# Performance work log

Hardware: AMD Instinct MI355X
Metric: run time of the kernel (lower is better)

The kernel has to match this reference:

```python
import jax, jax.numpy as jnp
import numpy as np

N = 13627
E = 504378
D = 500


def _seg_softmax(e, seg, n):
    m = jax.ops.segment_max(e, seg, num_segments=n)
    ex = jnp.exp(e - m[seg])
    s = jax.ops.segment_sum(ex, seg, num_segments=n)
    return ex / (s[seg] + 1e-16)


def _gatv2(x, src, dst, Wl, Wr, att, b, n):
    # PyG GATv2Conv (heads=1): message = Wl x_src; score uses Wl x_src + Wr x_dst
    xl = x @ Wl                                   # [N, F]
    xr = x @ Wr                                   # [N, F]
    e = jax.nn.leaky_relu(xl[src] + xr[dst], 0.2) @ att   # [E]
    a = _seg_softmax(e, dst, n)                   # segment softmax over targets
    out = jax.ops.segment_sum(a[:, None] * xl[src], dst, num_segments=n)
    return out + b


def setup_inputs() -> dict:
    key = jax.random.key(0)
    ks = jax.random.split(key, 24)
    s = 0.05
    inp = {
        'x': jax.random.normal(ks[0], (N, D), dtype=jnp.float32),
        'edge_index': jax.random.randint(ks[1], (2, E), 0, N),
        'neg_edge_index': jax.random.randint(ks[2], (2, E), 0, N),
        'Wl1': jax.random.normal(ks[3], (D, 300)) * s,
        'Wr1': jax.random.normal(ks[4], (D, 300)) * s,
        'att1': jax.random.normal(ks[5], (300,)) * s,
        'b1': jnp.zeros((300,)),
        'Wl2': jax.random.normal(ks[6], (300, 100)) * s,
        'Wr2': jax.random.normal(ks[7], (300, 100)) * s,
        'att2': jax.random.normal(ks[8], (100,)) * s,
        'b2': jnp.zeros((100,)),
        'Wl3': jax.random.normal(ks[9], (100, 1)) * s,
        'Wr3': jax.random.normal(ks[10], (100, 1)) * s,
        'att3': jax.random.normal(ks[11], (1,)) * s,
        'b3': jnp.zeros((1,)),
        'W_lin1': jax.random.normal(ks[12], (D, 100)) * s,
        'b_lin1': jnp.zeros((100,)),
        'W_lin2': jax.random.normal(ks[13], (D, 100)) * s,
        'b_lin2': jnp.zeros((100,)),
        'c1': jnp.array([0.5], dtype=jnp.float32),
        'c2': jnp.array([0.5], dtype=jnp.float32),
    }
    return inp


def reference(x, edge_index, neg_edge_index, Wl1, Wr1, att1, b1, Wl2, Wr2, att2, b2,
              Wl3, Wr3, att3, b3, W_lin1, b_lin1, W_lin2, b_lin2, c1, c2):
    # eval mode: dropout / dropout_adj are identity
    loops = jnp.arange(N)
    src = jnp.concatenate([edge_index[0], loops])   # GATv2Conv adds self loops
    dst = jnp.concatenate([edge_index[1], loops])

    h1 = jax.nn.relu(_gatv2(x, src, dst, Wl1, Wr1, att1, b1, N))
    h2 = jax.nn.relu(_gatv2(h1, src, dst, Wl2, Wr2, att2, b2, N))

    xo = h2 + jax.nn.relu(x @ W_lin1 + b_lin1)
    z = h2 + jax.nn.relu(x @ W_lin2 + b_lin2)

    # link-prediction reconstruction loss
    pos_s = jnp.sum(z[edge_index[0]] * z[edge_index[1]], axis=1)
    pos_loss = -jnp.mean(jnp.log(jax.nn.sigmoid(pos_s) + 1e-15))
    neg_s = jnp.sum(z[neg_edge_index[0]] * z[neg_edge_index[1]], axis=1)
    neg_loss = -jnp.mean(jnp.log(1.0 - jax.nn.sigmoid(neg_s) + 1e-15))
    r_loss = pos_loss + neg_loss

    out = _gatv2(xo, src, dst, Wl3, Wr3, att3, b3, N)   # [N, 1]
    return out, r_loss, c1, c2
```

## Files before the change

kernel.cpp:

```cpp
#include <hip/hip_runtime.h>
#include <hip/hip_bf16.h>

#define NODES 13627
#define DIM   500

typedef short short8 __attribute__((ext_vector_type(8)));
typedef float f32x4 __attribute__((ext_vector_type(4)));
typedef float floatx2 __attribute__((ext_vector_type(2)));

__device__ inline float wave_reduce_sum(float v) {
#pragma unroll
    for (int o = 32; o > 0; o >>= 1) v += __shfl_xor(v, o, 64);
    return v;
}

__device__ inline void store_v(float* p, float v) { *p = v; }
__device__ inline void store_v(__hip_bfloat16* p, float v) { *p = __float2bfloat16(v); }

__device__ inline float blo(unsigned w) { unsigned t = w << 16;        return __builtin_bit_cast(float, t); }
__device__ inline float bhi(unsigned w) { unsigned t = w & 0xffff0000u; return __builtin_bit_cast(float, t); }

__device__ inline unsigned char to_fp8(float v) {
    int r = __builtin_amdgcn_cvt_pk_fp8_f32(v, v, 0, false);
    return (unsigned char)(r & 0xff);
}

__device__ inline unsigned pk2bf(float a, float b) {
    unsigned la = (unsigned)__builtin_bit_cast(unsigned short, __float2bfloat16(a));
    unsigned hb = (unsigned)__builtin_bit_cast(unsigned short, __float2bfloat16(b));
    return la | (hb << 16);
}

template <int CTRL>
__device__ inline float dpp_add_step(float v) {
    int s = __builtin_amdgcn_update_dpp(0, __builtin_bit_cast(int, v), CTRL, 0xf, 0xf, true);
    return v + __builtin_bit_cast(float, s);
}
__device__ inline float quad16_reduce(float v) {
    v = dpp_add_step<0x128>(v);
    v = dpp_add_step<0x124>(v);
    v = dpp_add_step<0x4E>(v);
    v = dpp_add_step<0xB1>(v);
    return v;
}

struct b4 { __hip_bfloat16 a, b, c, d; };

__global__ __launch_bounds__(1024) void scan_kernel(int* __restrict__ cnt_cur,
                                                    int* __restrict__ off, int n) {
    __shared__ int wsum[16];
    const int tid = threadIdx.x, lane = tid & 63, w = tid >> 6;
    int carry = 0;
    for (int base = 0; base < n; base += 1024) {
        int i = base + tid;
        int v = (i < n) ? cnt_cur[i] : 0;
        int s = v;
#pragma unroll
        for (int o = 1; o < 64; o <<= 1) {
            int t = __shfl_up(s, o, 64);
            if (lane >= o) s += t;
        }
        if (lane == 63) wsum[w] = s;
        __syncthreads();
        if (w == 0 && lane < 16) {
            int x = wsum[lane];
            int sx = x;
#pragma unroll
            for (int o = 1; o < 16; o <<= 1) {
                int t = __shfl_up(sx, o, 64);
                if (lane >= o) sx += t;
            }
            wsum[lane] = sx;
        }
        __syncthreads();
        int wo = (w == 0) ? 0 : wsum[w - 1];
        int total = wsum[15];
        int excl = carry + wo + (s - v);
        if (i < n) { off[i] = excl; cnt_cur[i] = excl; }
        carry += total;
        __syncthreads();
    }
    if (tid == 0) off[n] = carry;
}

__global__ __launch_bounds__(256) void scatter_kernel(const int* __restrict__ src,
                                                      const int* __restrict__ dst,
                                                      int* __restrict__ cur,
                                                      int* __restrict__ ssrc, int E) {
    int i = blockIdx.x * blockDim.x + threadIdx.x;
    if (i < E) {
        int p = atomicAdd(&cur[dst[i]], 1);
        ssrc[p] = src[i];
    }
}

__global__ __launch_bounds__(256) void convert_all_kernel(
    const float* __restrict__ x,
    const float* __restrict__ Wl1, const float* __restrict__ Wr1,
    const float* __restrict__ Wl2, const float* __restrict__ Wr2,
    const float* __restrict__ Ws1, const float* __restrict__ Ws2,
    const float* __restrict__ bs1, const float* __restrict__ bs2,
    __hip_bfloat16* __restrict__ WcT, __hip_bfloat16* __restrict__ W2T,
    float* __restrict__ bcat, __hip_bfloat16* __restrict__ xb,
    const int* __restrict__ dst, int* __restrict__ cnt, int E, int M) {
    int i = blockIdx.x * 256 + threadIdx.x;
    if (i < E) atomicAdd(&cnt[dst[i]], 1);
    if (i < 327680) {
        int n = i >> 9, k = i & 511;
        float v = 0.f;
        if (k < 500) {
            if (n < 300) v = Wl1[k * 300 + n];
            else if (n < 600) v = Wr1[k * 300 + n - 300];
        }
        WcT[i] = __float2bfloat16(v);
    } else if (i < 409600) {
        int j = i - 327680;
        int n = j / 320, k = j - n * 320;
        float v = 0.f;
        if (k < 300) {
            if (n < 100) v = Wl2[k * 100 + n];
            else if (n < 200) v = Wr2[k * 100 + n - 100];
        }
        W2T[j] = __float2bfloat16(v);
    } else if (i < 540672) {
        int j = i - 409600;
        int n = j >> 9, k = j & 511;
        float v = 0.f;
        if (k < 500) {
            if (n < 100) v = Ws1[k * 100 + n];
            else if (n < 200) v = Ws2[k * 100 + n - 100];
        }
        WcT[327680 + j] = __float2bfloat16(v);
    } else if (i < 540928) {
        int n = i - 540672;
        float v = 0.f;
        if (n < 100) v = bs1[n];
        else if (n < 200) v = bs2[n - 100];
        bcat[n] = v;
    } else {
        int j = i - 540928;
        if (j >= M * 128) return;
        int m = j >> 7, k = (j & 127) << 2;
        b4 o;
        if (k < 500) {
            float4 v = *(const float4*)(x + (size_t)m * 500 + k);
            o.a = __float2bfloat16(v.x); o.b = __float2bfloat16(v.y);
            o.c = __float2bfloat16(v.z); o.d = __float2bfloat16(v.w);
        } else {
            o.a = o.b = o.c = o.d = __float2bfloat16(0.f);
        }
        *(b4*)(xb + (size_t)m * 512 + k) = o;
    }
}

template <int EPI, typename TC>
__global__ __launch_bounds__(256) void mfma_gemm(
    const __hip_bfloat16* __restrict__ A, const __hip_bfloat16* __restrict__ BT,
    TC* __restrict__ C, const float* __restrict__ bias, const float* __restrict__ h2,
    unsigned char* __restrict__ p8, __hip_bfloat16* __restrict__ pb,
    int M, int Kp, int Nn, int ldc) {
    __shared__ short AsF[8 * 64 * 8];
    __shared__ short BsF[4 * 64 * 8];
    const int t = threadIdx.x;
    const int w = t >> 6, lane = t & 63;
    const int c = t & 3, rr = t >> 2;

    const int nwg = gridDim.x * gridDim.y;
    int id = blockIdx.y * gridDim.x + blockIdx.x;
    {
        const int xcd = id & 7, idx = id >> 3;
        const int qq = nwg >> 3, r8 = nwg & 7;
        id = (xcd < r8 ? xcd * (qq + 1) : r8 * (qq + 1) + (xcd - r8) * qq) + idx;
    }
    const int m0 = (id / gridDim.x) * 128, n0 = (id % gridDim.x) * 64;

    f32x4 acc[2][4];
#pragma unroll
    for (int i = 0; i < 2; i++)
#pragma unroll
        for (int j = 0; j < 4; j++) acc[i][j] = (f32x4){0.f, 0.f, 0.f, 0.f};

    for (int k0 = 0; k0 < Kp; k0 += 32) {
#pragma unroll
        for (int r = 0; r < 2; r++) {
            int m = r * 64 + rr;
            int gm = m0 + m; if (gm >= M) gm = M - 1;
            float4 v = *(const float4*)(A + (size_t)gm * Kp + k0 + c * 8);
            int mi = m >> 4, sl = m & 15;
            *(float4*)(&AsF[(mi * 64 + c * 16 + sl) * 8]) = v;
        }
        {
            int n = rr;
            float4 v = *(const float4*)(BT + (size_t)(n0 + n) * Kp + k0 + c * 8);
            int ni = n >> 4, sl = n & 15;
            *(float4*)(&BsF[(ni * 64 + c * 16 + sl) * 8]) = v;
        }
        __syncthreads();
        short8 a0 = *(const short8*)(&AsF[((w * 2 + 0) * 64 + lane) * 8]);
        short8 a1 = *(const short8*)(&AsF[((w * 2 + 1) * 64 + lane) * 8]);
#pragma unroll
        for (int j = 0; j < 4; j++) {
            short8 b = *(const short8*)(&BsF[(j * 64 + lane) * 8]);
            acc[0][j] = __builtin_amdgcn_mfma_f32_16x16x32_bf16(a0, b, acc[0][j], 0, 0, 0);
            acc[1][j] = __builtin_amdgcn_mfma_f32_16x16x32_bf16(a1, b, acc[1][j], 0, 0, 0);
        }
        __syncthreads();
    }

    const int q = lane >> 4, sl = lane & 15;
#pragma unroll
    for (int i = 0; i < 2; i++) {
#pragma unroll
        for (int j = 0; j < 4; j++) {
#pragma unroll
            for (int reg = 0; reg < 4; reg++) {
                int gm = m0 + w * 32 + i * 16 + q * 4 + reg;
                int gn = n0 + j * 16 + sl;
                if (gm >= M) continue;
                float v = acc[i][j][reg];
                if constexpr (EPI == 1) {
                    if (gn < 300)       p8[(size_t)gm * 304 + gn] = to_fp8(v);
                    else if (gn < 600)  pb[(size_t)gm * 320 + (gn - 300)] = __float2bfloat16(v);
                    else if (gn < 620)  pb[(size_t)gm * 320 + (gn - 300)] = __float2bfloat16(0.f);
                    else if (gn < 624)  p8[(size_t)gm * 304 + (gn - 320)] = 0;
                    else if (gn >= 640 && gn < 840) {
                        int cn = gn - 640;
                        ((float*)C)[(size_t)gm * 200 + cn] = fmaxf(v + bias[cn], 0.f);
                    }
                } else if constexpr (EPI == 2) {
                    if (gn < 100)       p8[(size_t)gm * 112 + gn] = to_fp8(v);
                    else if (gn < 200)  pb[(size_t)gm * 128 + (gn - 100)] = __float2bfloat16(v);
                    else if (gn < 212)  p8[(size_t)gm * 112 + (gn - 100)] = 0;
                    else if (gn < 240)  pb[(size_t)gm * 128 + (gn - 112)] = __float2bfloat16(0.f);
                } else {
                    store_v(&C[(size_t)gm * ldc + gn], v);
                }
            }
        }
    }
}

__global__ __launch_bounds__(256) void skip_add_kernel(
    const float* __restrict__ pre, const float* __restrict__ h2,
    float* __restrict__ xo, unsigned char* __restrict__ z8, int n) {
    int tid = blockIdx.x * 256 + threadIdx.x;
    if (tid >= n * 128) return;
    int m = tid >> 7, k = tid & 127;
    if (k < 100) {
        float h = h2[(size_t)m * 100 + k];
        xo[(size_t)m * 100 + k] = pre[(size_t)m * 200 + k] + h;
        z8[(size_t)m * 128 + k] = to_fp8(pre[(size_t)m * 200 + 100 + k] + h);
    } else {
        z8[(size_t)m * 128 + k] = 0;
    }
}

template <int F, int NJ, int SL8, int SRB, int SOUT, int JSL, typename TOUT>
__global__ __launch_bounds__(64, 4) void gat_f8_kernel(
    const unsigned char* __restrict__ xl8, const __hip_bfloat16* __restrict__ xrb,
    const float* __restrict__ att, const float* __restrict__ bias,
    const int* __restrict__ off, const int* __restrict__ ssrc,
    TOUT* __restrict__ out, int n) {
    const int lane = threadIdx.x;
    const int sl = lane & 15, q = lane >> 4;
    const int wid = blockIdx.x;

    floatx2 attv[NJ * 2], xrv[NJ * 2], acc[NJ * 2];
    const unsigned* xru = (const unsigned*)xrb + (size_t)wid * (SRB / 2);
#pragma unroll
    for (int j = 0; j < NJ; j++) {
        const int f0 = sl * 4 + j * 64;
        if (f0 < F) {
            float4 a4 = *(const float4*)(att + f0);
            attv[j * 2 + 0] = (floatx2){a4.x, a4.y};
            attv[j * 2 + 1] = (floatx2){a4.z, a4.w};
        } else {
            attv[j * 2 + 0] = (floatx2){0.f, 0.f};
            attv[j * 2 + 1] = (floatx2){0.f, 0.f};
        }
        unsigned u0 = __builtin_nontemporal_load(xru + (f0 >> 1));
        unsigned u1 = __builtin_nontemporal_load(xru + (f0 >> 1) + 1);
        xrv[j * 2 + 0] = (floatx2){blo(u0), bhi(u0)};
        xrv[j * 2 + 1] = (floatx2){blo(u1), bhi(u1)};
        acc[j * 2 + 0] = (floatx2){0.f, 0.f};
        acc[j * 2 + 1] = (floatx2){0.f, 0.f};
    }

    const int s0 = off[wid], s1 = off[wid + 1];
    const int eb = s0 - 1;
    const int ee = s1;
    float den = 0.f;
    const int myoff = sl * 4;

    int srcB;
    unsigned u[NJ];
    {
        int eq0 = eb + q;
        int srcA = wid;
        if (eq0 >= s0 && eq0 < ee) srcA = __builtin_nontemporal_load(ssrc + eq0);
        int eq1 = eb + 4 + q;
        srcB = wid;
        if (eq1 >= s0 && eq1 < ee) srcB = __builtin_nontemporal_load(ssrc + eq1);
        const unsigned char* row = xl8 + (size_t)srcA * SL8;
#pragma unroll
        for (int j = 0; j < NJ; j++) {
            const bool ld = (j < NJ - 1) || (sl < JSL);
            u[j] = ld ? *(const unsigned*)(row + myoff + j * 64) : 0u;
        }
    }

    float p_pend = 0.f, gate = 0.f;
    unsigned u_pend[NJ];
#pragma unroll
    for (int j = 0; j < NJ; j++) u_pend[j] = 0u;

    for (int e0 = eb; e0 < ee; e0 += 4) {
        int srcC = wid;
        {
            int eq2 = e0 + 8 + q;
            if (eq2 >= s0 && eq2 < ee) srcC = __builtin_nontemporal_load(ssrc + eq2);
        }
        unsigned un[NJ];
        {
            const unsigned char* row1 = xl8 + (size_t)srcB * SL8;
#pragma unroll
            for (int j = 0; j < NJ; j++) {
                const bool ld = (j < NJ - 1) || (sl < JSL);
                un[j] = ld ? *(const unsigned*)(row1 + myoff + j * 64) : 0u;
            }
        }
        {
            float pp = quad16_reduce(p_pend);
            float ex = gate * __expf(pp);
            den += ex;
            floatx2 ex2 = (floatx2){ex, ex};
#pragma unroll
            for (int j = 0; j < NJ; j++) {
                floatx2 lo = __builtin_amdgcn_cvt_pk_f32_fp8((int)u_pend[j], false);
                floatx2 hi = __builtin_amdgcn_cvt_pk_f32_fp8((int)u_pend[j], true);
                acc[j * 2 + 0] += ex2 * lo;
                acc[j * 2 + 1] += ex2 * hi;
            }
        }
        {
            floatx2 p2 = (floatx2){0.f, 0.f};
#pragma unroll
            for (int j = 0; j < NJ; j++) {
                floatx2 lo = __builtin_amdgcn_cvt_pk_f32_fp8((int)u[j], false);
                floatx2 hi = __builtin_amdgcn_cvt_pk_f32_fp8((int)u[j], true);
                floatx2 s0v = lo + xrv[j * 2 + 0];
                floatx2 s1v = hi + xrv[j * 2 + 1];
                floatx2 g0 = __builtin_elementwise_max(s0v, 0.2f * s0v);
                floatx2 g1 = __builtin_elementwise_max(s1v, 0.2f * s1v);
                p2 += attv[j * 2 + 0] * g0;
                p2 += attv[j * 2 + 1] * g1;
            }
            p_pend = p2.x + p2.y;
            gate = ((e0 + q) < ee) ? 1.f : 0.f;
        }
#pragma unroll
        for (int j = 0; j < NJ; j++) { u_pend[j] = u[j]; u[j] = un[j]; }
        srcB = srcC;
    }
    {
        float pp = quad16_reduce(p_pend);
        float ex = gate * __expf(pp);
        den += ex;
        floatx2 ex2 = (floatx2){ex, ex};
#pragma unroll
        for (int j = 0; j < NJ; j++) {
            floatx2 lo = __builtin_amdgcn_cvt_pk_f32_fp8((int)u_pend[j], false);
            floatx2 hi = __builtin_amdgcn_cvt_pk_f32_fp8((int)u_pend[j], true);
            acc[j * 2 + 0] += ex2 * lo;
            acc[j * 2 + 1] += ex2 * hi;
        }
    }

    float* af = (float*)acc;
#pragma unroll
    for (int o = 16; o <= 32; o <<= 1) {
        den += __shfl_xor(den, o, 64);
#pragma unroll
        for (int i = 0; i < NJ * 4; i++) af[i] += __shfl_xor(af[i], o, 64);
    }

    if (q == 0) {
        const float inv = 1.f / (den + 1e-16f);
#pragma unroll
        for (int j = 0; j < NJ; j++) {
            const int f0 = sl * 4 + j * 64;
            if (f0 >= SOUT) continue;
            float r[4];
#pragma unroll
            for (int cc = 0; cc < 4; cc++) {
                const int f = f0 + cc;
                float v = 0.f;
                if (f < F) v = fmaxf(af[j * 4 + cc] * inv + bias[f], 0.f);
                r[cc] = v;
            }
            if constexpr (sizeof(TOUT) == 4) {
                *(float4*)((float*)out + (size_t)wid * SOUT + f0) =
                    make_float4(r[0], r[1], r[2], r[3]);
            } else {
                unsigned* op = (unsigned*)out + (size_t)wid * (SOUT / 2) + (f0 >> 1);
                op[0] = pk2bf(r[0], r[1]);
                op[1] = pk2bf(r[2], r[3]);
            }
        }
    }
}

__global__ __launch_bounds__(256) void gemm_vec1_kernel(
    const float* __restrict__ xo, const float* __restrict__ wl,
    const float* __restrict__ wr, float* __restrict__ xl3,
    float* __restrict__ xr3, int M, int ldx) {
    const int wid = blockIdx.x * 4 + (threadIdx.x >> 6);
    const int lane = threadIdx.x & 63;
    if (wid >= M) return;
    float a = 0.f, b = 0.f;
    for (int f = lane; f < 100; f += 64) {
        float v = xo[(size_t)wid * ldx + f];
        a += v * wl[f];
        b += v * wr[f];
    }
    a = wave_reduce_sum(a);
    b = wave_reduce_sum(b);
    if (lane == 0) { xl3[wid] = a; xr3[wid] = b; }
}

__global__ __launch_bounds__(256) void gat3_kernel(
    const float* __restrict__ xl3, const float* __restrict__ xr3,
    const float* __restrict__ att3, const float* __restrict__ b3,
    const int* __restrict__ off, const int* __restrict__ ssrc,
    float* __restrict__ out, int n) {
    const int wid = blockIdx.x * 4 + (threadIdx.x >> 6);
    const int lane = threadIdx.x & 63;
    if (wid >= n) return;
    const float xrv = xr3[wid];
    const float att = att3[0];
    float num = 0.f, den = 0.f;
    const int s0 = off[wid], s1 = off[wid + 1];
    for (int e = s0 - 1 + lane; e < s1; e += 64) {
        int src = (e < s0) ? wid : ssrc[e];
        float xlv = xl3[src];
        float t = xlv + xrv;
        float g = t > 0.f ? t : 0.2f * t;
        float ex = __expf(g * att);
        den += ex;
        num += ex * xlv;
    }
    num = wave_reduce_sum(num);
    den = wave_reduce_sum(den);
    if (lane == 0) out[wid] = num / (den + 1e-16f) + b3[0];
}

__global__ __launch_bounds__(256) void loss_kernel(
    const unsigned char* __restrict__ z8, const int* __restrict__ pos,
    const int* __restrict__ neg, float* __restrict__ part, int nb, int E) {
    const int lane = threadIdx.x & 63;
    const int sl = lane & 15;
    const int wlocal = threadIdx.x >> 6;
    const int q = lane >> 4;
    const int nq = gridDim.x * 16;
    const int qid = (blockIdx.x * 4 + wlocal) * 4 + q;
    const int total = 2 * E;
    float psum = 0.f, nsum = 0.f;

    for (int base = qid; base < total; base += 4 * nq) {
        uint2 au[4], bu[4];
        bool act[4], isN[4];
#pragma unroll
        for (int s = 0; s < 4; s++) {
            int it = base + s * nq;
            act[s] = it < total;
            int itc = act[s] ? it : 0;
            isN[s] = itc >= E;
            int e = isN[s] ? itc - E : itc;
            const int* ei = isN[s] ? neg : pos;
            int u = ei[e], v = ei[E + e];
            au[s] = *(const uint2*)(z8 + (size_t)u * 128 + sl * 8);
            bu[s] = *(const uint2*)(z8 + (size_t)v * 128 + sl * 8);
        }
#pragma unroll
        for (int s = 0; s < 4; s++) {
            floatx2 a0 = __builtin_amdgcn_cvt_pk_f32_fp8((int)au[s].x, false);
            floatx2 a1 = __builtin_amdgcn_cvt_pk_f32_fp8((int)au[s].x, true);
            floatx2 a2 = __builtin_amdgcn_cvt_pk_f32_fp8((int)au[s].y, false);
            floatx2 a3 = __builtin_amdgcn_cvt_pk_f32_fp8((int)au[s].y, true);
            floatx2 b0 = __builtin_amdgcn_cvt_pk_f32_fp8((int)bu[s].x, false);
            floatx2 b1 = __builtin_amdgcn_cvt_pk_f32_fp8((int)bu[s].x, true);
            floatx2 b2 = __builtin_amdgcn_cvt_pk_f32_fp8((int)bu[s].y, false);
            floatx2 b3 = __builtin_amdgcn_cvt_pk_f32_fp8((int)bu[s].y, true);
            float p = a0.x * b0.x + a0.y * b0.y + a1.x * b1.x + a1.y * b1.y
                    + a2.x * b2.x + a2.y * b2.y + a3.x * b3.x + a3.y * b3.y;
            p = quad16_reduce(p);
            if (sl == 0 && act[s]) {
                float sig = __builtin_amdgcn_rcpf(1.f + __expf(-p));
                if (isN[s]) nsum += __logf(1.f - sig + 1e-15f);
                else        psum += __logf(sig + 1e-15f);
            }
        }
    }
    float pw = wave_reduce_sum(psum);
    float nw = wave_reduce_sum(nsum);
    __shared__ float sp[4], sn[4];
    if (lane == 0) { sp[wlocal] = pw; sn[wlocal] = nw; }
    __syncthreads();
    if (threadIdx.x == 0) {
        part[blockIdx.x]      = sp[0] + sp[1] + sp[2] + sp[3];
        part[nb + blockIdx.x] = sn[0] + sn[1] + sn[2] + sn[3];
    }
}

__global__ __launch_bounds__(1024) void finalize_kernel(
    const float* __restrict__ part, int nb,
    const float* __restrict__ c1, const float* __restrict__ c2,
    float* __restrict__ out, int n, int E) {
    __shared__ float sp[16], sn[16];
    const int tid = threadIdx.x, lane = tid & 63, w = tid >> 6;
    float p = 0.f, q = 0.f;
    for (int i = tid; i < nb; i += 1024) { p += part[i]; q += part[nb + i]; }
    p = wave_reduce_sum(p);
    q = wave_reduce_sum(q);
    if (lane == 0) { sp[w] = p; sn[w] = q; }
    __syncthreads();
    if (tid == 0) {
        float tp = 0.f, tq = 0.f;
#pragma unroll
        for (int i = 0; i < 16; i++) { tp += sp[i]; tq += sn[i]; }
        out[n]     = -(tp + tq) / (float)E;
        out[n + 1] = c1[0];
        out[n + 2] = c2[0];
    }
}

extern "C" void kernel_launch(void* const* d_in, const int* in_sizes, int n_in,
                              void* d_out, int out_size, void* d_ws, size_t ws_size,
                              hipStream_t stream) {
    const float* x      = (const float*)d_in[0];
    const int*   ei     = (const int*)d_in[1];
    const int*   nei    = (const int*)d_in[2];
    const float* Wl1    = (const float*)d_in[3];
    const float* Wr1    = (const float*)d_in[4];
    const float* att1   = (const float*)d_in[5];
    const float* b1     = (const float*)d_in[6];
    const float* Wl2    = (const float*)d_in[7];
    const float* Wr2    = (const float*)d_in[8];
    const float* att2   = (const float*)d_in[9];
    const float* b2     = (const float*)d_in[10];
    const float* Wl3    = (const float*)d_in[11];
    const float* Wr3    = (const float*)d_in[12];
    const float* att3   = (const float*)d_in[13];
    const float* b3     = (const float*)d_in[14];
    const float* Wlin1  = (const float*)d_in[15];
    const float* blin1  = (const float*)d_in[16];
    const float* Wlin2  = (const float*)d_in[17];
    const float* blin2  = (const float*)d_in[18];
    const float* c1     = (const float*)d_in[19];
    const float* c2     = (const float*)d_in[20];
    float* out = (float*)d_out;

    const int E = in_sizes[1] / 2;
    const int N = NODES;
    const int LOSS_BLOCKS = 4096;

    char* ws = (char*)d_ws;
    unsigned char*  xl8  = (unsigned char*)(ws + 0);
    unsigned char*  xl28 = (unsigned char*)(ws + 0);
    __hip_bfloat16* xrb  = (__hip_bfloat16*)(ws + 4194304);
    __hip_bfloat16* xr2b = (__hip_bfloat16*)(ws + 4194304);
    float*          xo   = (float*)(ws + 4194304);
    unsigned char*  z8   = (unsigned char*)(ws + 9645312);
    __hip_bfloat16* h1b  = (__hip_bfloat16*)(ws + 12915712);
    float*          h2   = (float*)(ws + 12915712);
    __hip_bfloat16* xb   = (__hip_bfloat16*)(ws + 21637120);
    __hip_bfloat16* WcT  = (__hip_bfloat16*)(ws + 35591168);
    __hip_bfloat16* W2T  = (__hip_bfloat16*)(ws + 36508672);
    float*          bcat = (float*)(ws + 36672512);
    float*          xl3  = (float*)(ws + 36673536);
    float*          xr3  = (float*)(ws + 36728064);
    int*            ioff = (int*)(ws + 36782592);
    int*            cur  = (int*)(ws + 36837376);
    int*            ssrc = (int*)(ws + 36892160);
    float*          part = (float*)(ws + 38909952);
    float*          wpre = (float*)(ws + 39000064);

    hipMemsetAsync(cur, 0, sizeof(int) * N, stream);

    convert_all_kernel<<<(540928 + N * 128 + 255) / 256, 256, 0, stream>>>(
        x, Wl1, Wr1, Wl2, Wr2, Wlin1, Wlin2, blin1, blin2,
        WcT, W2T, bcat, xb, ei + E, cur, E, N);

    scan_kernel<<<1, 1024, 0, stream>>>(cur, ioff, N);
    scatter_kernel<<<(E + 255) / 256, 256, 0, stream>>>(ei, ei + E, cur, ssrc, E);

    mfma_gemm<1, float><<<dim3(14, 107), 256, 0, stream>>>(
        xb, WcT, wpre, bcat, nullptr, xl8, xrb, N, 512, 896, 200);
    gat_f8_kernel<300, 5, 304, 320, 320, 11, __hip_bfloat16>
        <<<N, 64, 0, stream>>>(xl8, xrb, att1, b1, ioff, ssrc, h1b, N);

    mfma_gemm<2, __hip_bfloat16><<<dim3(4, 107), 256, 0, stream>>>(
        h1b, W2T, (__hip_bfloat16*)nullptr, nullptr, nullptr, xl28, xr2b, N, 320, 256, 0);
    gat_f8_kernel<100, 2, 112, 128, 100, 9, float>
        <<<N, 64, 0, stream>>>(xl28, xr2b, att2, b2, ioff, ssrc, h2, N);

    skip_add_kernel<<<(N * 128 + 255) / 256, 256, 0, stream>>>(wpre, h2, xo, z8, N);

    loss_kernel<<<LOSS_BLOCKS, 256, 0, stream>>>(z8, ei, nei, part, LOSS_BLOCKS, E);

    gemm_vec1_kernel<<<(N + 3) / 4, 256, 0, stream>>>(xo, Wl3, Wr3, xl3, xr3, N, 100);
    gat3_kernel<<<(N + 3) / 4, 256, 0, stream>>>(xl3, xr3, att3, b3, ioff, ssrc, out, N);

    finalize_kernel<<<1, 1024, 0, stream>>>(part, LOSS_BLOCKS, c1, c2, out, N, E);
}
```

Baseline: 335.2 us.

## Fuse skip-add and layer-3 projection into GAT2 epilogue; merge finalize into gat3

The second GAT kernel's epilogue now computes the skip connections directly: it writes the fp8 z for the loss and reduces xo against Wl3/Wr3 to produce xl3/xr3. This removes the skip_add and gemm_vec1 kernels and the h2/xo round trips through memory. The loss finalize reduction moves into an extra last block of gat3_kernel, which removes one more launch. The fused epilogue does scalar per-element loads and stores of wpre and z8, and it runs only in the q==0 quarter of each wave.

```diff
diff --git a/kernel.cpp b/kernel.cpp
--- a/kernel.cpp
+++ b/kernel.cpp
@@ -240,27 +240,15 @@
     }
 }
 
-__global__ __launch_bounds__(256) void skip_add_kernel(
-    const float* __restrict__ pre, const float* __restrict__ h2,
-    float* __restrict__ xo, unsigned char* __restrict__ z8, int n) {
-    int tid = blockIdx.x * 256 + threadIdx.x;
-    if (tid >= n * 128) return;
-    int m = tid >> 7, k = tid & 127;
-    if (k < 100) {
-        float h = h2[(size_t)m * 100 + k];
-        xo[(size_t)m * 100 + k] = pre[(size_t)m * 200 + k] + h;
-        z8[(size_t)m * 128 + k] = to_fp8(pre[(size_t)m * 200 + 100 + k] + h);
-    } else {
-        z8[(size_t)m * 128 + k] = 0;
-    }
-}
-
-template <int F, int NJ, int SL8, int SRB, int SOUT, int JSL, typename TOUT>
+template <int F, int NJ, int SL8, int SRB, int SOUT, int JSL, typename TOUT, bool FUSE>
 __global__ __launch_bounds__(64, 4) void gat_f8_kernel(
     const unsigned char* __restrict__ xl8, const __hip_bfloat16* __restrict__ xrb,
     const float* __restrict__ att, const float* __restrict__ bias,
     const int* __restrict__ off, const int* __restrict__ ssrc,
-    TOUT* __restrict__ out, int n) {
+    TOUT* __restrict__ out,
+    const float* __restrict__ wpre, unsigned char* __restrict__ z8o,
+    float* __restrict__ xl3, float* __restrict__ xr3,
+    const float* __restrict__ wl3, const float* __restrict__ wr3, int n) {
     const int lane = threadIdx.x;
     const int sl = lane & 15, q = lane >> 4;
     const int wid = blockIdx.x;
@@ -386,53 +374,81 @@
 
     if (q == 0) {
         const float inv = 1.f / (den + 1e-16f);
-#pragma unroll
-        for (int j = 0; j < NJ; j++) {
-            const int f0 = sl * 4 + j * 64;
-            if (f0 >= SOUT) continue;
-            float r[4];
-#pragma unroll
-            for (int cc = 0; cc < 4; cc++) {
-                const int f = f0 + cc;
-                float v = 0.f;
-                if (f < F) v = fmaxf(af[j * 4 + cc] * inv + bias[f], 0.f);
-                r[cc] = v;
-            }
-            if constexpr (sizeof(TOUT) == 4) {
-                *(float4*)((float*)out + (size_t)wid * SOUT + f0) =
-                    make_float4(r[0], r[1], r[2], r[3]);
-            } else {
-                unsigned* op = (unsigned*)out + (size_t)wid * (SOUT / 2) + (f0 >> 1);
-                op[0] = pk2bf(r[0], r[1]);
-                op[1] = pk2bf(r[2], r[3]);
-            }
-        }
-    }
-}
-
-__global__ __launch_bounds__(256) void gemm_vec1_kernel(
-    const float* __restrict__ xo, const float* __restrict__ wl,
-    const float* __restrict__ wr, float* __restrict__ xl3,
-    float* __restrict__ xr3, int M, int ldx) {
-    const int wid = blockIdx.x * 4 + (threadIdx.x >> 6);
-    const int lane = threadIdx.x & 63;
-    if (wid >= M) return;
-    float a = 0.f, b = 0.f;
-    for (int f = lane; f < 100; f += 64) {
-        float v = xo[(size_t)wid * ldx + f];
-        a += v * wl[f];
-        b += v * wr[f];
-    }
-    a = wave_reduce_sum(a);
-    b = wave_reduce_sum(b);
-    if (lane == 0) { xl3[wid] = a; xr3[wid] = b; }
+        if constexpr (FUSE) {
+            float pl = 0.f, pr = 0.f;
+#pragma unroll
+            for (int j = 0; j < NJ; j++) {
+                const int f0 = sl * 4 + j * 64;
+#pragma unroll
+                for (int cc = 0; cc < 4; cc++) {
+                    const int f = f0 + cc;
+                    if (f < F) {
+                        float h2v = fmaxf(af[j * 4 + cc] * inv + bias[f], 0.f);
+                        float preA = wpre[(size_t)wid * 200 + f];
+                        float preB = wpre[(size_t)wid * 200 + 100 + f];
+                        float xov = preA + h2v;
+                        z8o[(size_t)wid * 128 + f] = to_fp8(preB + h2v);
+                        pl += xov * wl3[f];
+                        pr += xov * wr3[f];
+                    } else {
+                        z8o[(size_t)wid * 128 + f] = 0;
+                    }
+                }
+            }
+            pl = quad16_reduce(pl);
+            pr = quad16_reduce(pr);
+            if (sl == 0) { xl3[wid] = pl; xr3[wid] = pr; }
+        } else {
+#pragma unroll
+            for (int j = 0; j < NJ; j++) {
+                const int f0 = sl * 4 + j * 64;
+                if (f0 >= SOUT) continue;
+                float r[4];
+#pragma unroll
+                for (int cc = 0; cc < 4; cc++) {
+                    const int f = f0 + cc;
+                    float v = 0.f;
+                    if (f < F) v = fmaxf(af[j * 4 + cc] * inv + bias[f], 0.f);
+                    r[cc] = v;
+                }
+                if constexpr (sizeof(TOUT) == 4) {
+                    *(float4*)((float*)out + (size_t)wid * SOUT + f0) =
+                        make_float4(r[0], r[1], r[2], r[3]);
+                } else {
+                    unsigned* op = (unsigned*)out + (size_t)wid * (SOUT / 2) + (f0 >> 1);
+                    op[0] = pk2bf(r[0], r[1]);
+                    op[1] = pk2bf(r[2], r[3]);
+                }
+            }
+        }
+    }
 }
 
 __global__ __launch_bounds__(256) void gat3_kernel(
     const float* __restrict__ xl3, const float* __restrict__ xr3,
     const float* __restrict__ att3, const float* __restrict__ b3,
     const int* __restrict__ off, const int* __restrict__ ssrc,
-    float* __restrict__ out, int n) {
+    float* __restrict__ out, int n,
+    const float* __restrict__ part, int nb,
+    const float* __restrict__ c1, const float* __restrict__ c2, int E) {
+    __shared__ float sp[4], sn[4];
+    if (blockIdx.x == gridDim.x - 1) {
+        const int tid = threadIdx.x, lane = tid & 63, w = tid >> 6;
+        float p = 0.f, q2 = 0.f;
+        for (int i = tid; i < nb; i += 256) { p += part[i]; q2 += part[nb + i]; }
+        p = wave_reduce_sum(p);
+        q2 = wave_reduce_sum(q2);
+        if (lane == 0) { sp[w] = p; sn[w] = q2; }
+        __syncthreads();
+        if (tid == 0) {
+            float tp = sp[0] + sp[1] + sp[2] + sp[3];
+            float tq = sn[0] + sn[1] + sn[2] + sn[3];
+            out[n]     = -(tp + tq) / (float)E;
+            out[n + 1] = c1[0];
+            out[n + 2] = c2[0];
+        }
+        return;
+    }
     const int wid = blockIdx.x * 4 + (threadIdx.x >> 6);
     const int lane = threadIdx.x & 63;
     if (wid >= n) return;
@@ -509,28 +525,6 @@
     if (threadIdx.x == 0) {
         part[blockIdx.x]      = sp[0] + sp[1] + sp[2] + sp[3];
         part[nb + blockIdx.x] = sn[0] + sn[1] + sn[2] + sn[3];
-    }
-}
-
-__global__ __launch_bounds__(1024) void finalize_kernel(
-    const float* __restrict__ part, int nb,
-    const float* __restrict__ c1, const float* __restrict__ c2,
-    float* __restrict__ out, int n, int E) {
-    __shared__ float sp[16], sn[16];
-    const int tid = threadIdx.x, lane = tid & 63, w = tid >> 6;
-    float p = 0.f, q = 0.f;
-    for (int i = tid; i < nb; i += 1024) { p += part[i]; q += part[nb + i]; }
-    p = wave_reduce_sum(p);
-    q = wave_reduce_sum(q);
-    if (lane == 0) { sp[w] = p; sn[w] = q; }
-    __syncthreads();
-    if (tid == 0) {
-        float tp = 0.f, tq = 0.f;
-#pragma unroll
-        for (int i = 0; i < 16; i++) { tp += sp[i]; tq += sn[i]; }
-        out[n]     = -(tp + tq) / (float)E;
-        out[n + 1] = c1[0];
-        out[n + 2] = c2[0];
     }
 }
 
@@ -569,10 +563,8 @@
     unsigned char*  xl28 = (unsigned char*)(ws + 0);
     __hip_bfloat16* xrb  = (__hip_bfloat16*)(ws + 4194304);
     __hip_bfloat16* xr2b = (__hip_bfloat16*)(ws + 4194304);
-    float*          xo   = (float*)(ws + 4194304);
     unsigned char*  z8   = (unsigned char*)(ws + 9645312);
     __hip_bfloat16* h1b  = (__hip_bfloat16*)(ws + 12915712);
-    float*          h2   = (float*)(ws + 12915712);
     __hip_bfloat16* xb   = (__hip_bfloat16*)(ws + 21637120);
     __hip_bfloat16* WcT  = (__hip_bfloat16*)(ws + 35591168);
     __hip_bfloat16* W2T  = (__hip_bfloat16*)(ws + 36508672);
@@ -596,20 +588,18 @@
 
     mfma_gemm<1, float><<<dim3(14, 107), 256, 0, stream>>>(
         xb, WcT, wpre, bcat, nullptr, xl8, xrb, N, 512, 896, 200);
-    gat_f8_kernel<300, 5, 304, 320, 320, 11, __hip_bfloat16>
-        <<<N, 64, 0, stream>>>(xl8, xrb, att1, b1, ioff, ssrc, h1b, N);
+    gat_f8_kernel<300, 5, 304, 320, 320, 11, __hip_bfloat16, false>
+        <<<N, 64, 0, stream>>>(xl8, xrb, att1, b1, ioff, ssrc, h1b,
+                               nullptr, nullptr, nullptr, nullptr, nullptr, nullptr, N);
 
     mfma_gemm<2, __hip_bfloat16><<<dim3(4, 107), 256, 0, stream>>>(
         h1b, W2T, (__hip_bfloat16*)nullptr, nullptr, nullptr, xl28, xr2b, N, 320, 256, 0);
-    gat_f8_kernel<100, 2, 112, 128, 100, 9, float>
-        <<<N, 64, 0, stream>>>(xl28, xr2b, att2, b2, ioff, ssrc, h2, N);
-
-    skip_add_kernel<<<(N * 128 + 255) / 256, 256, 0, stream>>>(wpre, h2, xo, z8, N);
+    gat_f8_kernel<100, 2, 112, 128, 100, 9, float, true>
+        <<<N, 64, 0, stream>>>(xl28, xr2b, att2, b2, ioff, ssrc, (float*)nullptr,
+                               wpre, z8, xl3, xr3, Wl3, Wr3, N);
 
     loss_kernel<<<LOSS_BLOCKS, 256, 0, stream>>>(z8, ei, nei, part, LOSS_BLOCKS, E);
 
-    gemm_vec1_kernel<<<(N + 3) / 4, 256, 0, stream>>>(xo, Wl3, Wr3, xl3, xr3, N, 100);
-    gat3_kernel<<<(N + 3) / 4, 256, 0, stream>>>(xl3, xr3, att3, b3, ioff, ssrc, out, N);
-
-    finalize_kernel<<<1, 1024, 0, stream>>>(part, LOSS_BLOCKS, c1, c2, out, N, E);
-}
+    gat3_kernel<<<(N + 3) / 4 + 1, 256, 0, stream>>>(
+        xl3, xr3, att3, b3, ioff, ssrc, out, N, part, LOSS_BLOCKS, c1, c2, E);
+}
```

New measurement: 327.5 us. -2.3%, faster.
